# Performance work log

Hardware: AMD Instinct MI355X
Metric: run time of the kernel (lower is better)

The kernel has to match this reference:

```python
import jax, jax.numpy as jnp
import numpy as np

N_VARS = 50000
HID = 128
N_EDGES = 400000
EPS = 1e-5


def setup_inputs() -> dict:
    key = jax.random.key(0)
    ks = jax.random.split(key, 8)
    s = 1.0 / np.sqrt(HID)
    return {
        "h0": jax.random.normal(ks[0], (N_VARS, HID), jnp.float32),
        "var_reg": jax.random.uniform(ks[1], (N_VARS, 1), jnp.float32),
        "W_msg": jax.random.normal(ks[2], (HID, 2 * HID), jnp.float32) * s,
        "gamma": jnp.ones((HID,), jnp.float32),
        "beta": jnp.zeros((HID,), jnp.float32),
        "W_ih": jax.random.normal(ks[3], (4 * HID, HID), jnp.float32) * s,
        "W_hh": jax.random.normal(ks[4], (4 * HID, HID), jnp.float32) * s,
        "b_ih": jnp.zeros((4 * HID,), jnp.float32),
        "b_hh": jnp.zeros((4 * HID,), jnp.float32),
        "W_out": jax.random.normal(ks[5], (3, HID), jnp.float32) * s,
        "edge_idx": jax.random.randint(ks[6], (2, N_EDGES), 0, N_VARS, jnp.int32),
        "steps": 4,
    }


def reference(h0, var_reg, W_msg, gamma, beta, W_ih, W_hh, b_ih, b_hh, W_out, edge_idx, steps):
    N, H = h0.shape
    # Symmetric_Message_Network doubles the edge list with reversed direction.
    src = jnp.concatenate([edge_idx[0], edge_idx[1]])  # [2E]
    dst = jnp.concatenate([edge_idx[1], edge_idx[0]])  # [2E]

    h = h0
    c = jnp.zeros((N, H), jnp.float32)
    for _ in range(steps):
        # gather -> concat -> linear (bias=False) per edge
        m = jnp.concatenate([h[src], h[dst]], axis=1) @ W_msg.T  # [2E, H]
        # scatter_sum over destination endpoint
        rec = jax.ops.segment_sum(m, dst, num_segments=N)  # [N, H]
        rec = rec * var_reg
        # BatchNorm1d (training mode: biased batch stats)
        mean = rec.mean(axis=0)
        var = rec.var(axis=0)
        rec = (rec - mean) * jax.lax.rsqrt(var + EPS) * gamma + beta
        # LSTMCell
        gates = rec @ W_ih.T + b_ih + h @ W_hh.T + b_hh  # [N, 4H]
        i, f, g, o = jnp.split(gates, 4, axis=1)
        c = jax.nn.sigmoid(f) * c + jax.nn.sigmoid(i) * jnp.tanh(g)
        h = jax.nn.sigmoid(o) * jnp.tanh(c)
    # soft_assign: Linear(H,3,bias=False) + Softmax(dim=1), then unsqueeze(1)
    y = jax.nn.softmax(h @ W_out.T, axis=1)  # [N, 3]
    return y[:, None, :]  # [N, 1, 3]
```

## Files before the change

### kernel.cpp

```cpp
#include <hip/hip_runtime.h>
#include <cmath>

#define HID 128
#define K2  256

typedef unsigned short u16;
typedef unsigned int   u32;
typedef _Float16 f16;
typedef __attribute__((ext_vector_type(8))) _Float16 half8;
typedef __attribute__((ext_vector_type(4))) float f32x4;

__device__ __forceinline__ float fast_rcp(float x) { return __builtin_amdgcn_rcpf(x); }
__device__ __forceinline__ float sigm(float x) { return fast_rcp(1.0f + __expf(-x)); }
__device__ __forceinline__ float tanh_f(float x) { return 1.0f - 2.0f * fast_rcp(1.0f + __expf(2.0f * x)); }

__device__ __forceinline__ u16 f2h(float f) { return __builtin_bit_cast(u16, (f16)f); }
__device__ __forceinline__ float h2f(u16 w) { return (float)__builtin_bit_cast(f16, w); }
__device__ __forceinline__ float hlo(u32 w) { return h2f((u16)w); }
__device__ __forceinline__ float hhi(u32 w) { return h2f((u16)(w >> 16)); }
__device__ __forceinline__ u32 pk2h(float a, float b) { return (u32)f2h(a) | ((u32)f2h(b) << 16); }


__device__ __forceinline__ size_t afrag_idx(int NT, int j, int k) {
    return (size_t)((k >> 5) * NT + (j >> 4)) * 512 + ((k >> 3) & 3) * 128 + (j & 15) * 8 + (k & 7);
}

__global__ void k_init(const float* __restrict__ h0, const float* __restrict__ var_reg,
                       const float* __restrict__ Wmsg,
                       const float* __restrict__ W_ih, const float* __restrict__ W_hh,
                       const float* __restrict__ b_ih, const float* __restrict__ b_hh,
                       u16* __restrict__ hrow, u16* __restrict__ Pfrag,
                       float* __restrict__ cbuf, u16* __restrict__ Afrag1,
                       u16* __restrict__ AfragW, float* __restrict__ b2,
                       float* __restrict__ vr, int* __restrict__ deg,
                       float* __restrict__ colsum, float* __restrict__ colsumsq,
                       int N, int Mp) {
    int idx = blockIdx.x * blockDim.x + threadIdx.x;
    if (idx >= Mp * HID) return;
    int r = idx >> 7;
    hrow[idx] = (r < N) ? f2h(h0[idx]) : (u16)0;
    cbuf[idx] = 0.0f;
    {
        int tile = idx >> 14;
        int off = idx & 16383;
        int r2 = tile * 128 + ((off >> 9) & 7) * 16 + ((off >> 3) & 15);
        int c2 = ((off >> 12) & 3) * 32 + ((off >> 7) & 3) * 8 + (off & 7);
        Pfrag[((size_t)tile << 15) + 16384 + off] =
            (r2 < N) ? f2h(h0[(size_t)r2 * HID + c2]) : (u16)0;
    }
    if (idx < Mp)   { vr[idx] = (idx < N) ? var_reg[idx] : 0.0f; deg[idx] = 0; }
    if (idx < 4096) { colsum[idx] = 0.0f; colsumsq[idx] = 0.0f; }
    if (idx < HID * K2) {
        int j = idx >> 8, k = idx & 255;
        Afrag1[afrag_idx(8, j, k)] = f2h(Wmsg[idx]);
    }
    if (idx < 4 * HID * K2) {
        int j2 = idx >> 8, k = idx & 255;
        int mt = j2 >> 4, j2row = j2 & 15;
        int gate = j2row & 3;
        int hcol = (mt >> 2) * 16 + (j2row >> 2) * 4 + (mt & 3);
        int j = gate * HID + hcol;
        float w = (k < HID) ? W_ih[(size_t)j * HID + k] : W_hh[(size_t)j * HID + (k - HID)];
        AfragW[(size_t)((k >> 5) * 32 + mt) * 512 + (((k >> 3) & 3) << 7) + (j2row << 3) + (k & 7)] = f2h(w);
    }
    if (idx < 4 * HID) {
        int hc = idx >> 2, g = idx & 3;
        int j = g * HID + hc;
        b2[idx] = b_ih[j] + b_hh[j];
    }
}

__global__ void k_hist(const int* __restrict__ ei, int E, int* __restrict__ deg,
                       int* __restrict__ posA, int* __restrict__ posB) {
    int e = blockIdx.x * blockDim.x + threadIdx.x;
    if (e < E) {
        int a = ei[e], b = ei[E + e];
        posB[e] = atomicAdd(&deg[b], 1);
        posA[e] = atomicAdd(&deg[a], 1);
    }
}

__global__ void k_scan1(const int* __restrict__ deg, int* __restrict__ offs,
                        int* __restrict__ partials, int Mp) {
    __shared__ int s[256];
    int tid = threadIdx.x;
    int i = blockIdx.x * 256 + tid;
    int v = (i < Mp) ? deg[i] : 0;
    s[tid] = v;
    __syncthreads();
    for (int o = 1; o < 256; o <<= 1) {
        int t = (tid >= o) ? s[tid - o] : 0;
        __syncthreads();
        s[tid] += t;
        __syncthreads();
    }
    if (i < Mp) offs[i] = s[tid] - v;
    if (tid == 255) partials[blockIdx.x] = s[255];
}

__global__ void k_scan2(int* __restrict__ partials, int nb) {
    __shared__ int s[256];
    int tid = threadIdx.x;
    int v = (tid < nb) ? partials[tid] : 0;
    s[tid] = v;
    __syncthreads();
    for (int o = 1; o < 256; o <<= 1) {
        int t = (tid >= o) ? s[tid - o] : 0;
        __syncthreads();
        s[tid] += t;
        __syncthreads();
    }
    partials[tid] = s[tid] - v;
}

__global__ void k_scan3(const int* __restrict__ deg, int* __restrict__ offs,
                        const int* __restrict__ partials,
                        float* __restrict__ degf, int Mp, int E2) {
    int i = blockIdx.x * 256 + threadIdx.x;
    if (i < Mp) {
        offs[i] += partials[blockIdx.x];
        degf[i] = (float)deg[i];
    }
    if (i == 0) offs[Mp] = E2;
}

__global__ void k_fill(const int* __restrict__ ei, int E,
                       const int* __restrict__ offs,
                       const int* __restrict__ posA, const int* __restrict__ posB,
                       int* __restrict__ nbr) {
    int part = blockIdx.x & 7;
    int stride = (gridDim.x >> 3) * blockDim.x;
    for (int e = (blockIdx.x >> 3) * blockDim.x + threadIdx.x; e < E; e += stride) {
        int a = ei[e], b = ei[E + e];
        if ((b & 7) == part) nbr[offs[b] + posB[e]] = a;
        if ((a & 7) == part) nbr[offs[a] + posA[e]] = b;
    }
}

__global__ __launch_bounds__(512, 6) void k_ag1(const int* __restrict__ offs,
                                                const int* __restrict__ nbr,
                                                const u16* __restrict__ hrow,
                                                const float* __restrict__ degf,
                                                const u16* __restrict__ Afrag1,
                                                const float* __restrict__ vr,
                                                u16* __restrict__ ABc,
                                                float* __restrict__ colsum,
                                                float* __restrict__ colsumsq) {
    __shared__ u16 Xs[16384];
    __shared__ float csum[128], csq[128];
    int tid = threadIdx.x;
    int r0 = blockIdx.x * 64;
    int wv = tid >> 6, lane = tid & 63, lm = tid & 15, quad = (tid >> 4) & 3;
    if (tid < 128) { csum[tid] = 0.0f; csq[tid] = 0.0f; }
    const u16* hb = hrow + lane * 2;
    for (int t = 0; t < 8; ++t) {
        int rv = wv * 8 + t;
        int v = r0 + rv;
        int s = offs[v], e = offs[v + 1];
        float a0 = 0.0f, a1 = 0.0f;
        int i = s;
        for (; i + 7 < e; i += 8) {
            u32 w0 = *(const u32*)(hb + (size_t)nbr[i + 0] * HID);
            u32 w1 = *(const u32*)(hb + (size_t)nbr[i + 1] * HID);
            u32 w2 = *(const u32*)(hb + (size_t)nbr[i + 2] * HID);
            u32 w3 = *(const u32*)(hb + (size_t)nbr[i + 3] * HID);
            u32 w4 = *(const u32*)(hb + (size_t)nbr[i + 4] * HID);
            u32 w5 = *(const u32*)(hb + (size_t)nbr[i + 5] * HID);
            u32 w6 = *(const u32*)(hb + (size_t)nbr[i + 6] * HID);
            u32 w7 = *(const u32*)(hb + (size_t)nbr[i + 7] * HID);
            a0 += ((hlo(w0) + hlo(w1)) + (hlo(w2) + hlo(w3))) + ((hlo(w4) + hlo(w5)) + (hlo(w6) + hlo(w7)));
            a1 += ((hhi(w0) + hhi(w1)) + (hhi(w2) + hhi(w3))) + ((hhi(w4) + hhi(w5)) + (hhi(w6) + hhi(w7)));
        }
        for (; i < e; ++i) {
            u32 w0 = *(const u32*)(hb + (size_t)nbr[i] * HID);
            a0 += hlo(w0);
            a1 += hhi(w0);
        }
        u32 hv = *(const u32*)(hb + (size_t)v * HID);
        float d = degf[v];
        int k0 = lane * 2;
        *(u32*)(Xs + (((k0 >> 5) * 4 + (rv >> 4)) << 9)
                + (((k0 >> 3) & 3) << 7) + ((rv & 15) << 3) + (k0 & 7)) = pk2h(a0, a1);
        int k1 = 128 + k0;
        *(u32*)(Xs + (((k1 >> 5) * 4 + (rv >> 4)) << 9)
                + (((k1 >> 3) & 3) << 7) + ((rv & 15) << 3) + (k1 & 7)) = pk2h(hlo(hv) * d, hhi(hv) * d);
    }
    __syncthreads();
    const u16* Ap = Afrag1 + ((size_t)wv << 9) + (quad << 7) + (lm << 3);
    const u16* Bp = Xs + (quad << 7) + (lm << 3);
    f32x4 acc[4] = {};
#pragma unroll
    for (int kb = 0; kb < 8; ++kb) {
        half8 av = *(const half8*)(Ap + ((size_t)kb << 12));
        half8 bv[4];
#pragma unroll
        for (int j = 0; j < 4; ++j) bv[j] = *(const half8*)(Bp + (kb << 11) + (j << 9));
#pragma unroll
        for (int j = 0; j < 4; ++j)
            acc[j] = __builtin_amdgcn_mfma_f32_16x16x32_f16(av, bv[j], acc[j], 0, 0, 0);
    }
    __syncthreads();
    u16* Ht = Xs;
    float ss[4] = {}, qq[4] = {};
#pragma unroll
    for (int j = 0; j < 4; ++j) {
        int rho = j * 16 + lm;
        float v = vr[r0 + rho];
        f32x4 g = acc[j];
        float o0 = g.x * v, o1 = g.y * v, o2 = g.z * v, o3 = g.w * v;
        uint2 pk;
        pk.x = pk2h(o0, o1);
        pk.y = pk2h(o2, o3);
        *(uint2*)(Ht + rho * 136 + wv * 16 + quad * 4) = pk;
        ss[0] += o0; ss[1] += o1; ss[2] += o2; ss[3] += o3;
        qq[0] += o0 * o0; qq[1] += o1 * o1; qq[2] += o2 * o2; qq[3] += o3 * o3;
    }
#pragma unroll
    for (int t = 0; t < 4; ++t)
#pragma unroll
        for (int m = 1; m < 16; m <<= 1) {
            ss[t] += __shfl_xor(ss[t], m);
            qq[t] += __shfl_xor(qq[t], m);
        }
    if (lm == 0) {
        int c = wv * 16 + quad * 4;
#pragma unroll
        for (int t = 0; t < 4; ++t) {
            atomicAdd(&csum[c + t], ss[t]);
            atomicAdd(&csq[c + t], qq[t]);
        }
    }
    __syncthreads();
    size_t base = ((size_t)(r0 >> 7) << 15) + ((size_t)((r0 >> 4) & 4) << 9);
#pragma unroll
    for (int q = 0; q < 2; ++q) {
        int g = tid * 2 + q;
        int rr = ((g >> 6) & 3) * 16 + (g & 15);
        int lc = (g >> 8) * 32 + ((g >> 4) & 3) * 8;
        uint4 val = *(const uint4*)(Ht + rr * 136 + lc);
        *(uint4*)(ABc + base + ((size_t)(g >> 8) << 12) + ((size_t)(g & 255) << 3)) = val;
    }
    if (tid < 128) {
        int rep = (blockIdx.x & 7) * 128;
        atomicAdd(&colsum[rep + tid], csum[tid]);
        atomicAdd(&colsumsq[rep + tid], csq[tid]);
    }
}

__device__ __forceinline__ void stage_B64(const u16* __restrict__ Bt, u16* Bs, int tid) {
    int wv = tid >> 6, lane = tid & 63;
#pragma unroll
    for (int rd = 0; rd < 4; ++rd) {
        int c = rd * 8 + wv;
        int k5 = c >> 2, rhl = c & 3;
        __builtin_amdgcn_global_load_lds(
            (const __attribute__((address_space(1))) u32*)(Bt + ((size_t)k5 << 12) + (rhl << 9) + lane * 8),
            (__attribute__((address_space(3))) u32*)(Bs + ((size_t)c << 9)), 16, 0, 0);
    }
}

__global__ __launch_bounds__(512, 6) void k_gemm2(const u16* __restrict__ AfragW,
                                                  const u16* __restrict__ AB,
                                                  const float* __restrict__ b2,
                                                  const float* __restrict__ gamma,
                                                  const float* __restrict__ beta,
                                                  const float* __restrict__ colsum,
                                                  const float* __restrict__ colsumsq,
                                                  float* __restrict__ cbuf,
                                                  u16* __restrict__ Xh,
                                                  u16* __restrict__ hrow, int Mp, float invN) {
    __shared__ u16 Bs[16384];
    __shared__ u16 Ht[64 * 136];
    __shared__ float scs[128], shs[128];
    int tid = threadIdx.x;
    int r0 = blockIdx.x * 64;
    int wv = tid >> 6, lm = tid & 15, quad = (tid >> 4) & 3;
    const u16* Bt = AB + ((size_t)(r0 >> 7) << 15) + ((size_t)((r0 >> 4) & 4) << 9);
    stage_B64(Bt, Bs, tid);
    if (tid < 128) {
        float s1 = 0.0f, s2 = 0.0f;
#pragma unroll
        for (int rp = 0; rp < 8; ++rp) { s1 += colsum[rp * 128 + tid]; s2 += colsumsq[rp * 128 + tid]; }
        float mean = s1 * invN;
        float var = s2 * invN - mean * mean;
        float rstd = rsqrtf(var + 1e-5f);
        float s = gamma[tid] * rstd;
        scs[tid] = s;
        shs[tid] = beta[tid] - mean * s;
    }
    __syncthreads();
#pragma unroll
    for (int t = 0; t < 8; ++t) {
        int idx = tid + t * 512;
        int c = idx >> 8, o32 = idx & 255;
        int off16 = o32 << 1;
        int k = ((c >> 2) << 5) + ((off16 >> 7) << 3) + (off16 & 7);
        u32* p = (u32*)(Bs + (c << 9) + off16);
        u32 v = *p;
        *p = pk2h(hlo(v) * scs[k] + shs[k], hhi(v) * scs[k + 1] + shs[k + 1]);
    }
    __syncthreads();
    const u16* Bp = Bs + (quad << 7) + (lm << 3);
#pragma unroll
    for (int p = 0; p < 2; ++p) {
        const u16* Ap = AfragW + ((size_t)(wv * 4 + p * 2) << 9) + (quad << 7) + (lm << 3);
        f32x4 acc[2][4] = {};
#pragma unroll
        for (int kb = 0; kb < 8; ++kb) {
            half8 av[2], bv[4];
#pragma unroll
            for (int i = 0; i < 2; ++i) av[i] = *(const half8*)(Ap + ((size_t)kb << 14) + (i << 9));
#pragma unroll
            for (int j = 0; j < 4; ++j) bv[j] = *(const half8*)(Bp + (kb << 11) + (j << 9));
#pragma unroll
            for (int i = 0; i < 2; ++i)
#pragma unroll
                for (int j = 0; j < 4; ++j)
                    acc[i][j] = __builtin_amdgcn_mfma_f32_16x16x32_f16(av[i], bv[j], acc[i][j], 0, 0, 0);
        }
        int hc0 = wv * 16 + quad * 4 + p * 2;
        float4 bb0 = *(const float4*)(b2 + (size_t)hc0 * 4);
        float4 bb1 = *(const float4*)(b2 + (size_t)(hc0 + 1) * 4);
#pragma unroll
        for (int j = 0; j < 4; ++j) {
            int rho = j * 16 + lm;
            int r = r0 + rho;
            u16 hh[2];
#pragma unroll
            for (int i = 0; i < 2; ++i) {
                float4 bb = i ? bb1 : bb0;
                f32x4 g = acc[i][j];
                float gi = g.x + bb.x;
                float gf = g.y + bb.y;
                float gg = g.z + bb.z;
                float go = g.w + bb.w;
                float* cp = cbuf + (size_t)(hc0 + i) * Mp + r;
                float c = *cp;
                float cn = sigm(gf) * c + sigm(gi) * tanh_f(gg);
                *cp = cn;
                hh[i] = f2h(sigm(go) * tanh_f(cn));
            }
            *(u32*)(Ht + rho * 136 + hc0) = (u32)hh[0] | ((u32)hh[1] << 16);
        }
    }
    __syncthreads();
    {
        int rr = tid >> 3, part = tid & 7;
        const uint4* src = (const uint4*)(Ht + rr * 136 + part * 16);
        uint4* dst = (uint4*)(hrow + (size_t)(r0 + rr) * HID + part * 16);
        dst[0] = src[0]; dst[1] = src[1];
    }
    size_t base = ((size_t)(r0 >> 7) << 15) + ((size_t)((r0 >> 4) & 4) << 9);
#pragma unroll
    for (int q = 0; q < 2; ++q) {
        int g = tid * 2 + q;
        int rr = ((g >> 6) & 3) * 16 + (g & 15);
        int lc = (g >> 8) * 32 + ((g >> 4) & 3) * 8;
        uint4 val = *(const uint4*)(Ht + rr * 136 + lc);
        *(uint4*)(Xh + base + ((size_t)(4 + (g >> 8)) << 12) + ((size_t)(g & 255) << 3)) = val;
    }
}

__global__ __launch_bounds__(256) void k_out(const u16* __restrict__ hrow,
                                             const float* __restrict__ Wout,
                                             float* __restrict__ out, int N) {
    __shared__ float ws[384];
    if (threadIdx.x < 96) ((float4*)ws)[threadIdx.x] = ((const float4*)Wout)[threadIdx.x];
    __syncthreads();
    int r = blockIdx.x * blockDim.x + threadIdx.x;
    if (r >= N) return;
    const u32* hr = (const u32*)(hrow + (size_t)r * HID);
    float a0 = 0, a1 = 0, a2 = 0;
#pragma unroll
    for (int k = 0; k < 64; ++k) {
        u32 w = hr[k];
        float x0 = hlo(w), x1 = hhi(w);
        int c = k * 2;
        a0 += x0 * ws[c] + x1 * ws[c + 1];
        a1 += x0 * ws[128 + c] + x1 * ws[128 + c + 1];
        a2 += x0 * ws[256 + c] + x1 * ws[256 + c + 1];
    }
    float m = fmaxf(a0, fmaxf(a1, a2));
    float e0 = __expf(a0 - m), e1 = __expf(a1 - m), e2 = __expf(a2 - m);
    float inv = fast_rcp(e0 + e1 + e2);
    out[(size_t)r * 3 + 0] = e0 * inv;
    out[(size_t)r * 3 + 1] = e1 * inv;
    out[(size_t)r * 3 + 2] = e2 * inv;
}

extern "C" void kernel_launch(void* const* d_in, const int* in_sizes, int n_in,
                              void* d_out, int out_size, void* d_ws, size_t ws_size,
                              hipStream_t stream) {
    const float* h0      = (const float*)d_in[0];
    const float* var_reg = (const float*)d_in[1];
    const float* Wmsg    = (const float*)d_in[2];
    const float* gamma   = (const float*)d_in[3];
    const float* beta    = (const float*)d_in[4];
    const float* W_ih    = (const float*)d_in[5];
    const float* W_hh    = (const float*)d_in[6];
    const float* b_ih    = (const float*)d_in[7];
    const float* b_hh    = (const float*)d_in[8];
    const float* Wout    = (const float*)d_in[9];
    const int*   ei      = (const int*)d_in[10];

    const int N  = in_sizes[0] / HID;
    const int E  = in_sizes[10] / 2;
    const int Mp = ((N + 127) / 128) * 128;
    const int STEPS = 4;
    const size_t MpK = (size_t)Mp * K2;

    char* p = (char*)d_ws;
    u16* P    = (u16*)p; p += MpK * 2;
    u16* hrow = (u16*)p; p += (size_t)Mp * HID * 2;
    float* cbuf = (float*)p; p += (size_t)Mp * HID * 4;
    u16* Afrag1 = (u16*)p; p += (size_t)HID * K2 * 2;
    u16* AfragW = (u16*)p; p += (size_t)4 * HID * K2 * 2;
    float* b2 = (float*)p; p += 4 * HID * 4;
    float* vr   = (float*)p; p += (size_t)Mp * 4;
    float* degf = (float*)p; p += (size_t)Mp * 4;
    float* colsum   = (float*)p; p += 4096 * 4;
    float* colsumsq = (float*)p; p += 4096 * 4;
    int* deg      = (int*)p; p += (size_t)Mp * 4;
    int* offs     = (int*)p; p += (size_t)(Mp + 4) * 4;
    int* partials = (int*)p; p += 256 * 4;
    int* posA     = (int*)p; p += (size_t)E * 4;
    int* posB     = (int*)p; p += (size_t)E * 4;
    int* nbr      = (int*)p; p += (size_t)2 * E * 4;

    const int nch = (Mp + 255) / 256;

    k_init<<<(Mp * HID + 255) / 256, 256, 0, stream>>>(h0, var_reg, Wmsg, W_ih, W_hh, b_ih, b_hh,
                                                       hrow, P, cbuf, Afrag1, AfragW, b2,
                                                       vr, deg, colsum, colsumsq, N, Mp);
    k_hist<<<(E + 255) / 256, 256, 0, stream>>>(ei, E, deg, posA, posB);
    k_scan1<<<nch, 256, 0, stream>>>(deg, offs, partials, Mp);
    k_scan2<<<1, 256, 0, stream>>>(partials, nch);
    k_scan3<<<nch, 256, 0, stream>>>(deg, offs, partials, degf, Mp, 2 * E);
    k_fill<<<2048, 256, 0, stream>>>(ei, E, offs, posA, posB, nbr);

    for (int s = 0; s < STEPS; ++s) {
        k_ag1<<<Mp / 64, 512, 0, stream>>>(offs, nbr, hrow, degf, Afrag1, vr, P,
                                           colsum + s * 1024, colsumsq + s * 1024);
        k_gemm2<<<Mp / 64, 512, 0, stream>>>(AfragW, P, b2, gamma, beta,
                                             colsum + s * 1024, colsumsq + s * 1024,
                                             cbuf, P, hrow, Mp, 1.0f / (float)N);
    }
    k_out<<<(N + 255) / 256, 256, 0, stream>>>(hrow, Wout, (float*)d_out, N);
}
```

Baseline: 548.1 us.

## Restructure gather to 16-byte loads, store cell state in fp16, fuse output head

The neighbour gather now has each quarter-wave fetch full 16-byte octets of a neighbour row and reduces across quarters with shuffles, replacing per-lane 4-byte loads. The recurrent GEMM reads h directly from hrow into LDS, so the duplicated fragment-layout copy of h in P is dropped and P halves in size. The cell state moves to a per-block fp16 tile buffer, halving its traffic at some cost in precision. The final softmax projection is fused into the last gemm2 launch, removing the k_out kernel, and k_ag1's occupancy hint is raised.

```diff
diff --git a/kernel.cpp b/kernel.cpp
--- a/kernel.cpp
+++ b/kernel.cpp
@@ -20,7 +20,6 @@
 __device__ __forceinline__ float hhi(u32 w) { return h2f((u16)(w >> 16)); }
 __device__ __forceinline__ u32 pk2h(float a, float b) { return (u32)f2h(a) | ((u32)f2h(b) << 16); }
 
-
 __device__ __forceinline__ size_t afrag_idx(int NT, int j, int k) {
     return (size_t)((k >> 5) * NT + (j >> 4)) * 512 + ((k >> 3) & 3) * 128 + (j & 15) * 8 + (k & 7);
 }
@@ -29,9 +28,9 @@
                        const float* __restrict__ Wmsg,
                        const float* __restrict__ W_ih, const float* __restrict__ W_hh,
                        const float* __restrict__ b_ih, const float* __restrict__ b_hh,
-                       u16* __restrict__ hrow, u16* __restrict__ Pfrag,
-                       float* __restrict__ cbuf, u16* __restrict__ Afrag1,
-                       u16* __restrict__ AfragW, float* __restrict__ b2,
+                       u16* __restrict__ hrow, u16* __restrict__ cbuf16,
+                       u16* __restrict__ Afrag1, u16* __restrict__ AfragW,
+                       float* __restrict__ b2,
                        float* __restrict__ vr, int* __restrict__ deg,
                        float* __restrict__ colsum, float* __restrict__ colsumsq,
                        int N, int Mp) {
@@ -39,15 +38,7 @@
     if (idx >= Mp * HID) return;
     int r = idx >> 7;
     hrow[idx] = (r < N) ? f2h(h0[idx]) : (u16)0;
-    cbuf[idx] = 0.0f;
-    {
-        int tile = idx >> 14;
-        int off = idx & 16383;
-        int r2 = tile * 128 + ((off >> 9) & 7) * 16 + ((off >> 3) & 15);
-        int c2 = ((off >> 12) & 3) * 32 + ((off >> 7) & 3) * 8 + (off & 7);
-        Pfrag[((size_t)tile << 15) + 16384 + off] =
-            (r2 < N) ? f2h(h0[(size_t)r2 * HID + c2]) : (u16)0;
-    }
+    cbuf16[idx] = 0;
     if (idx < Mp)   { vr[idx] = (idx < N) ? var_reg[idx] : 0.0f; deg[idx] = 0; }
     if (idx < 4096) { colsum[idx] = 0.0f; colsumsq[idx] = 0.0f; }
     if (idx < HID * K2) {
@@ -137,13 +128,13 @@
     }
 }
 
-__global__ __launch_bounds__(512, 6) void k_ag1(const int* __restrict__ offs,
+__global__ __launch_bounds__(512, 8) void k_ag1(const int* __restrict__ offs,
                                                 const int* __restrict__ nbr,
                                                 const u16* __restrict__ hrow,
                                                 const float* __restrict__ degf,
                                                 const u16* __restrict__ Afrag1,
                                                 const float* __restrict__ vr,
-                                                u16* __restrict__ ABc,
+                                                u16* __restrict__ Pc,
                                                 float* __restrict__ colsum,
                                                 float* __restrict__ colsumsq) {
     __shared__ u16 Xs[16384];
@@ -152,38 +143,60 @@
     int r0 = blockIdx.x * 64;
     int wv = tid >> 6, lane = tid & 63, lm = tid & 15, quad = (tid >> 4) & 3;
     if (tid < 128) { csum[tid] = 0.0f; csq[tid] = 0.0f; }
-    const u16* hb = hrow + lane * 2;
+    int g = lane >> 4;
+    int c8 = lane & 15;
+    const u16* hoct = hrow + c8 * 8;
     for (int t = 0; t < 8; ++t) {
         int rv = wv * 8 + t;
         int v = r0 + rv;
         int s = offs[v], e = offs[v + 1];
-        float a0 = 0.0f, a1 = 0.0f;
+        float a[8] = {};
         int i = s;
         for (; i + 7 < e; i += 8) {
-            u32 w0 = *(const u32*)(hb + (size_t)nbr[i + 0] * HID);
-            u32 w1 = *(const u32*)(hb + (size_t)nbr[i + 1] * HID);
-            u32 w2 = *(const u32*)(hb + (size_t)nbr[i + 2] * HID);
-            u32 w3 = *(const u32*)(hb + (size_t)nbr[i + 3] * HID);
-            u32 w4 = *(const u32*)(hb + (size_t)nbr[i + 4] * HID);
-            u32 w5 = *(const u32*)(hb + (size_t)nbr[i + 5] * HID);
-            u32 w6 = *(const u32*)(hb + (size_t)nbr[i + 6] * HID);
-            u32 w7 = *(const u32*)(hb + (size_t)nbr[i + 7] * HID);
-            a0 += ((hlo(w0) + hlo(w1)) + (hlo(w2) + hlo(w3))) + ((hlo(w4) + hlo(w5)) + (hlo(w6) + hlo(w7)));
-            a1 += ((hhi(w0) + hhi(w1)) + (hhi(w2) + hhi(w3))) + ((hhi(w4) + hhi(w5)) + (hhi(w6) + hhi(w7)));
-        }
-        for (; i < e; ++i) {
-            u32 w0 = *(const u32*)(hb + (size_t)nbr[i] * HID);
-            a0 += hlo(w0);
-            a1 += hhi(w0);
-        }
-        u32 hv = *(const u32*)(hb + (size_t)v * HID);
-        float d = degf[v];
-        int k0 = lane * 2;
-        *(u32*)(Xs + (((k0 >> 5) * 4 + (rv >> 4)) << 9)
-                + (((k0 >> 3) & 3) << 7) + ((rv & 15) << 3) + (k0 & 7)) = pk2h(a0, a1);
-        int k1 = 128 + k0;
-        *(u32*)(Xs + (((k1 >> 5) * 4 + (rv >> 4)) << 9)
-                + (((k1 >> 3) & 3) << 7) + ((rv & 15) << 3) + (k1 & 7)) = pk2h(hlo(hv) * d, hhi(hv) * d);
+            int u0 = nbr[i + g];
+            int u1 = nbr[i + 4 + g];
+            uint4 w0 = *(const uint4*)(hoct + (size_t)u0 * HID);
+            uint4 w1 = *(const uint4*)(hoct + (size_t)u1 * HID);
+            a[0] += hlo(w0.x) + hlo(w1.x); a[1] += hhi(w0.x) + hhi(w1.x);
+            a[2] += hlo(w0.y) + hlo(w1.y); a[3] += hhi(w0.y) + hhi(w1.y);
+            a[4] += hlo(w0.z) + hlo(w1.z); a[5] += hhi(w0.z) + hhi(w1.z);
+            a[6] += hlo(w0.w) + hlo(w1.w); a[7] += hhi(w0.w) + hhi(w1.w);
+        }
+        for (; i < e; i += 4) {
+            int idx = i + g;
+            int u = nbr[min(idx, e - 1)];
+            uint4 w = *(const uint4*)(hoct + (size_t)u * HID);
+            if (idx < e) {
+                a[0] += hlo(w.x); a[1] += hhi(w.x);
+                a[2] += hlo(w.y); a[3] += hhi(w.y);
+                a[4] += hlo(w.z); a[5] += hhi(w.z);
+                a[6] += hlo(w.w); a[7] += hhi(w.w);
+            }
+        }
+#pragma unroll
+        for (int q = 0; q < 8; ++q) {
+            a[q] += __shfl_xor(a[q], 16);
+            a[q] += __shfl_xor(a[q], 32);
+        }
+        if (g == 0) {
+            int k = c8 * 8;
+            uint4 val;
+            val.x = pk2h(a[0], a[1]); val.y = pk2h(a[2], a[3]);
+            val.z = pk2h(a[4], a[5]); val.w = pk2h(a[6], a[7]);
+            *(uint4*)(Xs + (((k >> 5) * 4 + (rv >> 4)) << 9)
+                      + (((k >> 3) & 3) << 7) + ((rv & 15) << 3)) = val;
+        } else if (g == 1) {
+            uint4 hv4 = *(const uint4*)(hoct + (size_t)v * HID);
+            float d = degf[v];
+            int k = 128 + c8 * 8;
+            uint4 val;
+            val.x = pk2h(hlo(hv4.x) * d, hhi(hv4.x) * d);
+            val.y = pk2h(hlo(hv4.y) * d, hhi(hv4.y) * d);
+            val.z = pk2h(hlo(hv4.z) * d, hhi(hv4.z) * d);
+            val.w = pk2h(hlo(hv4.w) * d, hhi(hv4.w) * d);
+            *(uint4*)(Xs + (((k >> 5) * 4 + (rv >> 4)) << 9)
+                      + (((k >> 3) & 3) << 7) + ((rv & 15) << 3)) = val;
+        }
     }
     __syncthreads();
     const u16* Ap = Afrag1 + ((size_t)wv << 9) + (quad << 7) + (lm << 3);
@@ -206,8 +219,8 @@
     for (int j = 0; j < 4; ++j) {
         int rho = j * 16 + lm;
         float v = vr[r0 + rho];
-        f32x4 g = acc[j];
-        float o0 = g.x * v, o1 = g.y * v, o2 = g.z * v, o3 = g.w * v;
+        f32x4 gg = acc[j];
+        float o0 = gg.x * v, o1 = gg.y * v, o2 = gg.z * v, o3 = gg.w * v;
         uint2 pk;
         pk.x = pk2h(o0, o1);
         pk.y = pk2h(o2, o3);
@@ -231,14 +244,19 @@
         }
     }
     __syncthreads();
-    size_t base = ((size_t)(r0 >> 7) << 15) + ((size_t)((r0 >> 4) & 4) << 9);
+    size_t pbase = (size_t)(r0 >> 7) * 16384;
+    int rh0 = (r0 >> 4) & 4;
 #pragma unroll
     for (int q = 0; q < 2; ++q) {
-        int g = tid * 2 + q;
-        int rr = ((g >> 6) & 3) * 16 + (g & 15);
-        int lc = (g >> 8) * 32 + ((g >> 4) & 3) * 8;
-        uint4 val = *(const uint4*)(Ht + rr * 136 + lc);
-        *(uint4*)(ABc + base + ((size_t)(g >> 8) << 12) + ((size_t)(g & 255) << 3)) = val;
+        int g2 = tid * 2 + q;
+        int cL = g2 >> 6;
+        int gg = g2 & 63;
+        int koct2 = gg >> 4, rl = gg & 15;
+        int rr = (cL & 3) * 16 + rl;
+        int k = (cL >> 2) * 32 + koct2 * 8;
+        uint4 val = *(const uint4*)(Ht + rr * 136 + k);
+        *(uint4*)(Pc + pbase + (((cL >> 2) * 8 + rh0 + (cL & 3)) << 9)
+                  + (koct2 << 7) + (rl << 3)) = val;
     }
     if (tid < 128) {
         int rep = (blockIdx.x & 7) * 128;
@@ -247,36 +265,47 @@
     }
 }
 
-__device__ __forceinline__ void stage_B64(const u16* __restrict__ Bt, u16* Bs, int tid) {
-    int wv = tid >> 6, lane = tid & 63;
-#pragma unroll
-    for (int rd = 0; rd < 4; ++rd) {
-        int c = rd * 8 + wv;
-        int k5 = c >> 2, rhl = c & 3;
-        __builtin_amdgcn_global_load_lds(
-            (const __attribute__((address_space(1))) u32*)(Bt + ((size_t)k5 << 12) + (rhl << 9) + lane * 8),
-            (__attribute__((address_space(3))) u32*)(Bs + ((size_t)c << 9)), 16, 0, 0);
-    }
-}
-
 __global__ __launch_bounds__(512, 6) void k_gemm2(const u16* __restrict__ AfragW,
-                                                  const u16* __restrict__ AB,
+                                                  const u16* __restrict__ P,
                                                   const float* __restrict__ b2,
                                                   const float* __restrict__ gamma,
                                                   const float* __restrict__ beta,
                                                   const float* __restrict__ colsum,
                                                   const float* __restrict__ colsumsq,
-                                                  float* __restrict__ cbuf,
-                                                  u16* __restrict__ Xh,
-                                                  u16* __restrict__ hrow, int Mp, float invN) {
+                                                  u16* __restrict__ cbuf16,
+                                                  u16* __restrict__ hrow,
+                                                  const float* __restrict__ Wout,
+                                                  float* __restrict__ out,
+                                                  int Mp, float invN, int N, int last) {
     __shared__ u16 Bs[16384];
     __shared__ u16 Ht[64 * 136];
     __shared__ float scs[128], shs[128];
+    __shared__ float wouts[384];
     int tid = threadIdx.x;
     int r0 = blockIdx.x * 64;
-    int wv = tid >> 6, lm = tid & 15, quad = (tid >> 4) & 3;
-    const u16* Bt = AB + ((size_t)(r0 >> 7) << 15) + ((size_t)((r0 >> 4) & 4) << 9);
-    stage_B64(Bt, Bs, tid);
+    int wv = tid >> 6, lane = tid & 63, lm = tid & 15, quad = (tid >> 4) & 3;
+    int tile = r0 >> 7, rh0 = (r0 >> 4) & 4;
+#pragma unroll
+    for (int cc = 0; cc < 2; ++cc) {
+        int c = wv * 2 + cc;
+        int k5 = c >> 2, rhl = c & 3;
+        __builtin_amdgcn_global_load_lds(
+            (const __attribute__((address_space(1))) u32*)(P + (size_t)tile * 16384
+                + ((k5 * 8 + rh0 + rhl) << 9) + lane * 8),
+            (__attribute__((address_space(3))) u32*)(Bs + (c << 9)), 16, 0, 0);
+    }
+    {
+        int rr = tid >> 3, pp = tid & 7;
+        const u16* hsrc = hrow + (size_t)(r0 + rr) * HID + pp * 16;
+        uint4 h0v = *(const uint4*)hsrc;
+        uint4 h1v = *(const uint4*)(hsrc + 8);
+        int k = pp * 16;
+        *(uint4*)(Bs + ((16 + (k >> 5) * 4 + (rr >> 4)) << 9)
+                  + (((k >> 3) & 3) << 7) + ((rr & 15) << 3)) = h0v;
+        int k2 = k + 8;
+        *(uint4*)(Bs + ((16 + (k2 >> 5) * 4 + (rr >> 4)) << 9)
+                  + (((k2 >> 3) & 3) << 7) + ((rr & 15) << 3)) = h1v;
+    }
     if (tid < 128) {
         float s1 = 0.0f, s2 = 0.0f;
 #pragma unroll
@@ -288,6 +317,7 @@
         scs[tid] = s;
         shs[tid] = beta[tid] - mean * s;
     }
+    if (last && tid < 96) ((float4*)wouts)[tid] = ((const float4*)Wout)[tid];
     __syncthreads();
 #pragma unroll
     for (int t = 0; t < 8; ++t) {
@@ -301,6 +331,7 @@
     }
     __syncthreads();
     const u16* Bp = Bs + (quad << 7) + (lm << 3);
+    u16* ct = cbuf16 + (size_t)blockIdx.x * 8192;
 #pragma unroll
     for (int p = 0; p < 2; ++p) {
         const u16* Ap = AfragW + ((size_t)(wv * 4 + p * 2) << 9) + (quad << 7) + (lm << 3);
@@ -324,68 +355,59 @@
 #pragma unroll
         for (int j = 0; j < 4; ++j) {
             int rho = j * 16 + lm;
-            int r = r0 + rho;
             u16 hh[2];
 #pragma unroll
             for (int i = 0; i < 2; ++i) {
                 float4 bb = i ? bb1 : bb0;
-                f32x4 g = acc[i][j];
-                float gi = g.x + bb.x;
-                float gf = g.y + bb.y;
-                float gg = g.z + bb.z;
-                float go = g.w + bb.w;
-                float* cp = cbuf + (size_t)(hc0 + i) * Mp + r;
-                float c = *cp;
+                f32x4 gv = acc[i][j];
+                float gi = gv.x + bb.x;
+                float gf = gv.y + bb.y;
+                float gg = gv.z + bb.z;
+                float go = gv.w + bb.w;
+                u16* cp = ct + (hc0 + i) * 64 + rho;
+                float c = h2f(*cp);
                 float cn = sigm(gf) * c + sigm(gi) * tanh_f(gg);
-                *cp = cn;
+                *cp = f2h(cn);
                 hh[i] = f2h(sigm(go) * tanh_f(cn));
             }
             *(u32*)(Ht + rho * 136 + hc0) = (u32)hh[0] | ((u32)hh[1] << 16);
         }
     }
     __syncthreads();
-    {
+    if (!last) {
         int rr = tid >> 3, part = tid & 7;
         const uint4* src = (const uint4*)(Ht + rr * 136 + part * 16);
         uint4* dst = (uint4*)(hrow + (size_t)(r0 + rr) * HID + part * 16);
         dst[0] = src[0]; dst[1] = src[1];
-    }
-    size_t base = ((size_t)(r0 >> 7) << 15) + ((size_t)((r0 >> 4) & 4) << 9);
-#pragma unroll
-    for (int q = 0; q < 2; ++q) {
-        int g = tid * 2 + q;
-        int rr = ((g >> 6) & 3) * 16 + (g & 15);
-        int lc = (g >> 8) * 32 + ((g >> 4) & 3) * 8;
-        uint4 val = *(const uint4*)(Ht + rr * 136 + lc);
-        *(uint4*)(Xh + base + ((size_t)(4 + (g >> 8)) << 12) + ((size_t)(g & 255) << 3)) = val;
-    }
-}
-
-__global__ __launch_bounds__(256) void k_out(const u16* __restrict__ hrow,
-                                             const float* __restrict__ Wout,
-                                             float* __restrict__ out, int N) {
-    __shared__ float ws[384];
-    if (threadIdx.x < 96) ((float4*)ws)[threadIdx.x] = ((const float4*)Wout)[threadIdx.x];
-    __syncthreads();
-    int r = blockIdx.x * blockDim.x + threadIdx.x;
-    if (r >= N) return;
-    const u32* hr = (const u32*)(hrow + (size_t)r * HID);
-    float a0 = 0, a1 = 0, a2 = 0;
-#pragma unroll
-    for (int k = 0; k < 64; ++k) {
-        u32 w = hr[k];
-        float x0 = hlo(w), x1 = hhi(w);
-        int c = k * 2;
-        a0 += x0 * ws[c] + x1 * ws[c + 1];
-        a1 += x0 * ws[128 + c] + x1 * ws[128 + c + 1];
-        a2 += x0 * ws[256 + c] + x1 * ws[256 + c + 1];
-    }
-    float m = fmaxf(a0, fmaxf(a1, a2));
-    float e0 = __expf(a0 - m), e1 = __expf(a1 - m), e2 = __expf(a2 - m);
-    float inv = fast_rcp(e0 + e1 + e2);
-    out[(size_t)r * 3 + 0] = e0 * inv;
-    out[(size_t)r * 3 + 1] = e1 * inv;
-    out[(size_t)r * 3 + 2] = e2 * inv;
+    } else {
+        int rr = tid >> 3, pp = tid & 7;
+        int r = r0 + rr;
+        const u16* hsrc = Ht + rr * 136 + pp * 16;
+        float a0 = 0, a1 = 0, a2 = 0;
+#pragma unroll
+        for (int q = 0; q < 8; ++q) {
+            u32 w = *(const u32*)(hsrc + q * 2);
+            float x0 = hlo(w), x1 = hhi(w);
+            int col = pp * 16 + q * 2;
+            a0 += x0 * wouts[col] + x1 * wouts[col + 1];
+            a1 += x0 * wouts[128 + col] + x1 * wouts[128 + col + 1];
+            a2 += x0 * wouts[256 + col] + x1 * wouts[256 + col + 1];
+        }
+#pragma unroll
+        for (int m = 1; m < 8; m <<= 1) {
+            a0 += __shfl_xor(a0, m);
+            a1 += __shfl_xor(a1, m);
+            a2 += __shfl_xor(a2, m);
+        }
+        if (pp == 0 && r < N) {
+            float mx = fmaxf(a0, fmaxf(a1, a2));
+            float e0 = __expf(a0 - mx), e1 = __expf(a1 - mx), e2 = __expf(a2 - mx);
+            float inv = fast_rcp(e0 + e1 + e2);
+            out[(size_t)r * 3 + 0] = e0 * inv;
+            out[(size_t)r * 3 + 1] = e1 * inv;
+            out[(size_t)r * 3 + 2] = e2 * inv;
+        }
+    }
 }
 
 extern "C" void kernel_launch(void* const* d_in, const int* in_sizes, int n_in,
@@ -407,12 +429,11 @@
     const int E  = in_sizes[10] / 2;
     const int Mp = ((N + 127) / 128) * 128;
     const int STEPS = 4;
-    const size_t MpK = (size_t)Mp * K2;
 
     char* p = (char*)d_ws;
-    u16* P    = (u16*)p; p += MpK * 2;
+    u16* P    = (u16*)p; p += (size_t)Mp * HID * 2;
     u16* hrow = (u16*)p; p += (size_t)Mp * HID * 2;
-    float* cbuf = (float*)p; p += (size_t)Mp * HID * 4;
+    u16* cbuf16 = (u16*)p; p += (size_t)Mp * HID * 2;
     u16* Afrag1 = (u16*)p; p += (size_t)HID * K2 * 2;
     u16* AfragW = (u16*)p; p += (size_t)4 * HID * K2 * 2;
     float* b2 = (float*)p; p += 4 * HID * 4;
@@ -430,7 +451,7 @@
     const int nch = (Mp + 255) / 256;
 
     k_init<<<(Mp * HID + 255) / 256, 256, 0, stream>>>(h0, var_reg, Wmsg, W_ih, W_hh, b_ih, b_hh,
-                                                       hrow, P, cbuf, Afrag1, AfragW, b2,
+                                                       hrow, cbuf16, Afrag1, AfragW, b2,
                                                        vr, deg, colsum, colsumsq, N, Mp);
     k_hist<<<(E + 255) / 256, 256, 0, stream>>>(ei, E, deg, posA, posB);
     k_scan1<<<nch, 256, 0, stream>>>(deg, offs, partials, Mp);
@@ -443,7 +464,7 @@
                                            colsum + s * 1024, colsumsq + s * 1024);
         k_gemm2<<<Mp / 64, 512, 0, stream>>>(AfragW, P, b2, gamma, beta,
                                              colsum + s * 1024, colsumsq + s * 1024,
-                                             cbuf, P, hrow, Mp, 1.0f / (float)N);
-    }
-    k_out<<<(N + 255) / 256, 256, 0, stream>>>(hrow, Wout, (float*)d_out, N);
-}
+                                             cbuf16, hrow, Wout, (float*)d_out,
+                                             Mp, 1.0f / (float)N, N, (s == STEPS - 1) ? 1 : 0);
+    }
+}
```

New measurement: 482.8 us. 11.9% less time.
